# Performance work log

Measured on AMD Instinct MI355X. Metric: run time of the kernel, lower is better.

The kernel has to match this reference:

```python
import jax, jax.numpy as jnp
import numpy as np

N_STEPS = 4   # wavelet steps
N_LIFT = 2    # lifting steps per wavelet step
B, N = 512, 65536
TAPS = 3


def setup_inputs() -> dict:
    key = jax.random.key(0)
    k1, k2, k3 = jax.random.split(key, 3)
    x = jax.random.normal(k1, (B, N), dtype=jnp.float32)
    # torch inits these to zeros; use small random values to exercise the math
    P_coeffs = jax.random.normal(k2, (N_STEPS * N_LIFT, TAPS), dtype=jnp.float32) * 0.1
    U_coeffs = jax.random.normal(k3, (N_STEPS * N_LIFT, TAPS), dtype=jnp.float32) * 0.1
    return {"x": x, "P_coeffs": P_coeffs, "U_coeffs": U_coeffs}


def _cconv(x, h):
    # circular convolution: y[n] = sum_k h[k] * x[(n-k) mod N]; h has 3 taps
    return sum(h[k] * jnp.roll(x, k, axis=-1) for k in range(TAPS))


def reference(x, P_coeffs, U_coeffs):
    zs = []
    lowpass = x
    for j in range(N_STEPS):
        # LazyWavelet: even/odd polyphase split
        evens = lowpass[:, 0::2]
        odds = lowpass[:, 1::2]
        # Lifting steps
        for k in range(N_LIFT):
            i = j * N_LIFT + k
            detail = odds - _cconv(evens, P_coeffs[i])
            average = evens + _cconv(detail, U_coeffs[i])
            evens, odds = average, detail
        # Wavelet.forward keeps coeffs[:,0] (average) as z, recurses on coeffs[:,1] (detail)
        zs.append(evens)
        lowpass = odds
    zs.append(lowpass)
    return tuple(zs)
```

## Files before the change

kernel.cpp:

```cpp
#include <hip/hip_runtime.h>

#define BS    128
#define CHUNK 2048
#define HALO  256
#define NN    65536
#define LDSF  2304

template<int M, int NP>
__device__ __forceinline__ void lift_read(const float* __restrict__ A, int inOff,
                                          int t, float* __restrict__ in) {
  const int p0 = M * t - 8;
#pragma unroll
  for (int i = 0; i < M + 8; ++i) {
    int p = p0 + i;
    p = p < 0 ? 0 : (p >= NP ? NP - 1 : p);
    float2 v = *(const float2*)&A[inOff + 2 * p];
    in[2 * i] = v.x;
    in[2 * i + 1] = v.y;
  }
}

template<int M, int NP>
__device__ __forceinline__ void lift_write(float* __restrict__ A, int avgOff,
                                           int detOff, int t,
                                           const float* __restrict__ in,
                                           const float* __restrict__ P6,
                                           const float* __restrict__ U6) {
  const float P0 = P6[0], P1 = P6[1], P2 = P6[2], P3 = P6[3], P4 = P6[4], P5 = P6[5];
  const float U0 = U6[0], U1 = U6[1], U2 = U6[2], U3 = U6[3], U4 = U6[4], U5 = U6[5];
  const int p0 = M * t - 8;
  float e1 = 0, e2 = 0, d1 = 0, d2 = 0, a1 = 0, a2 = 0, f1 = 0, f2 = 0;
#pragma unroll
  for (int i = 0; i < M + 8; ++i) {
    float e0 = in[2 * i], o0 = in[2 * i + 1];
    float d0 = o0 - (P0 * e0 + P1 * e1 + P2 * e2);
    float a0 = e0 + (U0 * d0 + U1 * d1 + U2 * d2);
    float f0 = d0 - (P3 * a0 + P4 * a1 + P5 * a2);
    float b0 = a0 + (U3 * f0 + U4 * f1 + U5 * f2);
    if (i >= 8) {
      int p = p0 + i;
      if (p < NP) { A[avgOff + p] = b0; A[detOff + p] = f0; }
    }
    e2 = e1; e1 = e0; d2 = d1; d1 = d0; a2 = a1; a1 = a0; f2 = f1; f1 = f0;
  }
}

__global__ __launch_bounds__(BS, 8)
void wavelet_fused_kernel(const float* __restrict__ x,
                          const float* __restrict__ Pc,
                          const float* __restrict__ Uc,
                          float* __restrict__ out) {
  __shared__ __align__(16) float A[LDSF];

  const int tid  = threadIdx.x;
  const int wave = tid >> 6;
  const int lane = tid & 63;
  const int cx   = blockIdx.x;
  const int row  = blockIdx.y;
  const int S    = cx * CHUNK;

  {
    const float4* x4 = (const float4*)(x + (size_t)row * NN);
    const int base4 = ((S - HALO) & (NN - 1)) >> 2;
    for (int s = wave; s < 9; s += 2) {
      const float4* g = &x4[(base4 + s * 64 + lane) & (NN / 4 - 1)];
      __builtin_amdgcn_global_load_lds(
          (const __attribute__((address_space(1))) void*)g,
          (__attribute__((address_space(3))) void*)&A[s * 256], 16, 0, 0);
    }
  }
  __syncthreads();

  float4* z0 = (float4*)out + (size_t)row * 8192 + (S >> 3);
  float4* z1 = (float4*)out + 4194304 + row * 4096 + (S >> 4);
  float4* z2 = (float4*)out + 6291456 + row * 2048 + (S >> 5);
  float4* z3 = (float4*)out + 7340032 + row * 1024 + (S >> 6);
  float4* z4 = (float4*)out + 7864320 + row * 1024 + (S >> 6);

  {
    float in0[34];
    lift_read<9, 1152>(A, 0, tid, in0);
    __syncthreads();
    lift_write<9, 1152>(A, 0, 1152, tid, in0, Pc, Uc);
  }
  __syncthreads();

  float in1[34];
  if (tid < 64) {
    lift_read<9, 576>(A, 1152, tid, in1);
  } else {
    const int t = tid - 64;
#pragma unroll
    for (int k = 0; k < 4; ++k) z0[t + 64 * k] = *(const float4*)&A[128 + 4 * (t + 64 * k)];
  }
  __syncthreads();
  if (tid < 64) lift_write<9, 576>(A, 1152, 1728, tid, in1, Pc + 6, Uc + 6);
  __syncthreads();

  float in2[26];
  if (tid < 64) {
    lift_read<5, 288>(A, 1728, tid, in2);
  } else {
    const int t = tid - 64;
#pragma unroll
    for (int k = 0; k < 2; ++k) z1[t + 64 * k] = *(const float4*)&A[1216 + 4 * (t + 64 * k)];
  }
  __syncthreads();
  if (tid < 64) lift_write<5, 288>(A, 1728, 2016, tid, in2, Pc + 12, Uc + 12);
  __syncthreads();

  float in3[22];
  if (tid < 64) {
    lift_read<3, 144>(A, 2016, tid, in3);
  } else {
    const int t = tid - 64;
    z2[t] = *(const float4*)&A[1760 + 4 * t];
  }
  __syncthreads();
  if (tid < 64) lift_write<3, 144>(A, 2016, 2160, tid, in3, Pc + 18, Uc + 18);
  __syncthreads();

  if (tid < 32)                     z3[tid]      = *(const float4*)&A[2032 + 4 * tid];
  else if (tid >= 64 && tid < 96)   z4[tid - 64] = *(const float4*)&A[2176 + 4 * (tid - 64)];
}

extern "C" void kernel_launch(void* const* d_in, const int* in_sizes, int n_in,
                              void* d_out, int out_size, void* d_ws, size_t ws_size,
                              hipStream_t stream) {
  const float* x  = (const float*)d_in[0];
  const float* Pc = (const float*)d_in[1];
  const float* Uc = (const float*)d_in[2];
  float* out = (float*)d_out;

  dim3 grid(NN / CHUNK, 512, 1);
  dim3 block(BS, 1, 1);
  wavelet_fused_kernel<<<grid, block, 0, stream>>>(x, Pc, Uc, out);
}
```

Before: 49.74 us.

## Double chunk size per block and trim halo recomputation in lifting

Each block now handles a 4096-sample chunk with 256 threads instead of 2048 with 128. The fixed 256-sample halo is therefore amortised over twice as much useful output, which cuts redundant halo loads and recompute. Thread counts per lifting level are retuned (242/121/61/55 active threads). The warm-up iterations in the lift are restructured so only the needed dependency chain is computed instead of full iterations. In exchange, LDS use per block rises to about 17KB and more threads sit idle in the deeper levels.

```diff
diff --git a/kernel.cpp b/kernel.cpp
--- a/kernel.cpp
+++ b/kernel.cpp
@@ -1,14 +1,15 @@
 #include <hip/hip_runtime.h>
 
-#define BS    128
-#define CHUNK 2048
+#define BS    256
+#define CHUNK 4096
 #define HALO  256
 #define NN    65536
-#define LDSF  2304
+#define LDSF  4352
 
-template<int M, int NP>
+template<int M, int T, int NP>
 __device__ __forceinline__ void lift_read(const float* __restrict__ A, int inOff,
                                           int t, float* __restrict__ in) {
+  if (t >= T) return;
   const int p0 = M * t - 8;
 #pragma unroll
   for (int i = 0; i < M + 8; ++i) {
@@ -20,27 +21,37 @@
   }
 }
 
-template<int M, int NP>
+template<int M, int T, int NP>
 __device__ __forceinline__ void lift_write(float* __restrict__ A, int avgOff,
                                            int detOff, int t,
                                            const float* __restrict__ in,
                                            const float* __restrict__ P6,
                                            const float* __restrict__ U6) {
+  if (t >= T) return;
   const float P0 = P6[0], P1 = P6[1], P2 = P6[2], P3 = P6[3], P4 = P6[4], P5 = P6[5];
   const float U0 = U6[0], U1 = U6[1], U2 = U6[2], U3 = U6[3], U4 = U6[4], U5 = U6[5];
   const int p0 = M * t - 8;
-  float e1 = 0, e2 = 0, d1 = 0, d2 = 0, a1 = 0, a2 = 0, f1 = 0, f2 = 0;
+  float dd[6], aa[4], ff[2];
 #pragma unroll
-  for (int i = 0; i < M + 8; ++i) {
+  for (int k = 0; k < 6; ++k)
+    dd[k] = in[2 * (k + 2) + 1] - (P0 * in[2 * (k + 2)] + P1 * in[2 * (k + 1)] + P2 * in[2 * k]);
+#pragma unroll
+  for (int k = 0; k < 4; ++k)
+    aa[k] = in[2 * (k + 4)] + (U0 * dd[k + 2] + U1 * dd[k + 1] + U2 * dd[k]);
+#pragma unroll
+  for (int k = 0; k < 2; ++k)
+    ff[k] = dd[k + 4] - (P3 * aa[k + 2] + P4 * aa[k + 1] + P5 * aa[k]);
+  float e1 = in[14], e2 = in[12];
+  float d1 = dd[5], d2 = dd[4], a1 = aa[3], a2 = aa[2], f1 = ff[1], f2 = ff[0];
+#pragma unroll
+  for (int i = 8; i < M + 8; ++i) {
     float e0 = in[2 * i], o0 = in[2 * i + 1];
     float d0 = o0 - (P0 * e0 + P1 * e1 + P2 * e2);
     float a0 = e0 + (U0 * d0 + U1 * d1 + U2 * d2);
     float f0 = d0 - (P3 * a0 + P4 * a1 + P5 * a2);
     float b0 = a0 + (U3 * f0 + U4 * f1 + U5 * f2);
-    if (i >= 8) {
-      int p = p0 + i;
-      if (p < NP) { A[avgOff + p] = b0; A[detOff + p] = f0; }
-    }
+    int p = p0 + i;
+    if (p < NP) { A[avgOff + p] = b0; A[detOff + p] = f0; }
     e2 = e1; e1 = e0; d2 = d1; d1 = d0; a2 = a1; a1 = a0; f2 = f1; f1 = f0;
   }
 }
@@ -62,7 +73,7 @@
   {
     const float4* x4 = (const float4*)(x + (size_t)row * NN);
     const int base4 = ((S - HALO) & (NN - 1)) >> 2;
-    for (int s = wave; s < 9; s += 2) {
+    for (int s = wave; s < 17; s += 4) {
       const float4* g = &x4[(base4 + s * 64 + lane) & (NN / 4 - 1)];
       __builtin_amdgcn_global_load_lds(
           (const __attribute__((address_space(1))) void*)g,
@@ -79,49 +90,50 @@
 
   {
     float in0[34];
-    lift_read<9, 1152>(A, 0, tid, in0);
+    lift_read<9, 242, 2176>(A, 0, tid, in0);
     __syncthreads();
-    lift_write<9, 1152>(A, 0, 1152, tid, in0, Pc, Uc);
+    lift_write<9, 242, 2176>(A, 0, 2176, tid, in0, Pc, Uc);
   }
   __syncthreads();
 
   float in1[34];
-  if (tid < 64) {
-    lift_read<9, 576>(A, 1152, tid, in1);
+  if (tid >= 128) {
+    const float4* s = (const float4*)(A + 128);
+    const int t = tid - 128;
+#pragma unroll
+    for (int k = 0; k < 4; ++k) z0[t + 128 * k] = s[t + 128 * k];
   } else {
-    const int t = tid - 64;
-#pragma unroll
-    for (int k = 0; k < 4; ++k) z0[t + 64 * k] = *(const float4*)&A[128 + 4 * (t + 64 * k)];
+    lift_read<9, 121, 1088>(A, 2176, tid, in1);
   }
   __syncthreads();
-  if (tid < 64) lift_write<9, 576>(A, 1152, 1728, tid, in1, Pc + 6, Uc + 6);
+  lift_write<9, 121, 1088>(A, 2176, 3264, tid, in1, Pc + 6, Uc + 6);
   __syncthreads();
 
-  float in2[26];
-  if (tid < 64) {
-    lift_read<5, 288>(A, 1728, tid, in2);
+  float in2[34];
+  if (tid >= 128) {
+    const float4* s = (const float4*)(A + 2240);
+    const int t = tid - 128;
+#pragma unroll
+    for (int k = 0; k < 2; ++k) z1[t + 128 * k] = s[t + 128 * k];
   } else {
-    const int t = tid - 64;
-#pragma unroll
-    for (int k = 0; k < 2; ++k) z1[t + 64 * k] = *(const float4*)&A[1216 + 4 * (t + 64 * k)];
+    lift_read<9, 61, 544>(A, 3264, tid, in2);
   }
   __syncthreads();
-  if (tid < 64) lift_write<5, 288>(A, 1728, 2016, tid, in2, Pc + 12, Uc + 12);
+  lift_write<9, 61, 544>(A, 3264, 3808, tid, in2, Pc + 12, Uc + 12);
   __syncthreads();
 
-  float in3[22];
-  if (tid < 64) {
-    lift_read<3, 144>(A, 2016, tid, in3);
+  float in3[26];
+  if (tid >= 128) {
+    z2[tid - 128] = ((const float4*)(A + 3296))[tid - 128];
   } else {
-    const int t = tid - 64;
-    z2[t] = *(const float4*)&A[1760 + 4 * t];
+    lift_read<5, 55, 272>(A, 3808, tid, in3);
   }
   __syncthreads();
-  if (tid < 64) lift_write<3, 144>(A, 2016, 2160, tid, in3, Pc + 18, Uc + 18);
+  lift_write<5, 55, 272>(A, 3808, 4080, tid, in3, Pc + 18, Uc + 18);
   __syncthreads();
 
-  if (tid < 32)                     z3[tid]      = *(const float4*)&A[2032 + 4 * tid];
-  else if (tid >= 64 && tid < 96)   z4[tid - 64] = *(const float4*)&A[2176 + 4 * (tid - 64)];
+  if (tid < 64)        z3[tid] = ((const float4*)(A + 3824))[tid];
+  else if (tid < 128)  z4[tid - 64] = ((const float4*)(A + 4096))[tid - 64];
 }
 
 extern "C" void kernel_launch(void* const* d_in, const int* in_sizes, int n_in,
```

New measurement: 50.05 us. No clear change (+0.6%).
